# Performance work log

Hardware: AMD Instinct MI355X
Metric: run time of the kernel (lower is better)

Reference implementation:

```python
import jax, jax.numpy as jnp
import numpy as np

N_EMBD = 1024
N_HEAD = 16
HEAD_DIM = N_EMBD // N_HEAD


def setup_inputs() -> dict:
    key = jax.random.key(0)
    ks = jax.random.split(key, 5)
    B, T = 4, 2048
    s = 0.02
    return {
        "x": jax.random.normal(ks[0], (B, T, N_EMBD), dtype=jnp.float32),
        "w_qkv": jax.random.normal(ks[1], (N_EMBD, 3 * N_EMBD), dtype=jnp.float32) * s,
        "b_qkv": jnp.zeros((3 * N_EMBD,), dtype=jnp.float32),
        "w_out": jax.random.normal(ks[2], (N_EMBD, N_EMBD), dtype=jnp.float32) * s,
        "b_out": jnp.zeros((N_EMBD,), dtype=jnp.float32),
    }


def reference(x, w_qkv, b_qkv, w_out, b_out):
    # Eval-mode forward (dropout disabled), matching the torch module's math.
    B, T, C = x.shape
    qkv = x @ w_qkv + b_qkv                      # [B,T,3C]
    q, k, v = jnp.split(qkv, 3, axis=-1)
    def heads(t):
        return t.reshape(B, T, N_HEAD, HEAD_DIM).transpose(0, 2, 1, 3)  # [B,H,T,D]
    q, k, v = heads(q), heads(k), heads(v)
    scores = jnp.einsum("bhtd,bhsd->bhts", q, k) / jnp.sqrt(jnp.float32(HEAD_DIM))
    causal = jnp.tril(jnp.ones((T, T), dtype=bool))
    scores = jnp.where(causal[None, None], scores, -jnp.inf)
    attn = jax.nn.softmax(scores, axis=-1)       # [B,H,T,T]
    y = jnp.einsum("bhts,bhsd->bhtd", attn, v)   # [B,H,T,D]
    y = y.transpose(0, 2, 1, 3).reshape(B, T, C)
    return y @ w_out + b_out
```

## Files before the change

kernel.cpp:

```cpp
#include <hip/hip_runtime.h>
#include <hip/hip_bf16.h>

#define TSEQ 2048
#define CEMB 1024

typedef __attribute__((ext_vector_type(8))) short bf16x8;
typedef __attribute__((ext_vector_type(4))) float f32x4;
typedef __attribute__((ext_vector_type(16))) float f32x16;
typedef __attribute__((ext_vector_type(4))) int i32x4;

__device__ __forceinline__ unsigned short f2bf(float f){
  return __builtin_bit_cast(unsigned short, __float2bfloat16(f));
}

__global__ void k_cvt_bf16(const float* __restrict__ in, unsigned short* __restrict__ out, int n4){
  int i = blockIdx.x * blockDim.x + threadIdx.x;
  if (i >= n4) return;
  const float4 v = reinterpret_cast<const float4*>(in)[i];
  ushort4 o;
  o.x = f2bf(v.x); o.y = f2bf(v.y); o.z = f2bf(v.z); o.w = f2bf(v.w);
  reinterpret_cast<ushort4*>(out)[i] = o;
}

__global__ void k_transpose_bf16(const float* __restrict__ w, unsigned short* __restrict__ wT, int K, int N){
  __shared__ unsigned short tile[32][33];
  const int n0 = blockIdx.x * 32, k0 = blockIdx.y * 32;
  const int tx = threadIdx.x & 31, ty = threadIdx.x >> 5;
  #pragma unroll
  for (int r = 0; r < 4; ++r){
    int k = ty * 4 + r;
    tile[k][tx] = f2bf(w[(size_t)(k0 + k) * N + n0 + tx]);
  }
  __syncthreads();
  #pragma unroll
  for (int r = 0; r < 4; ++r){
    int n = ty * 4 + r;
    wT[(size_t)(n0 + n) * K + k0 + tx] = tile[tx][n];
  }
}

__global__ __launch_bounds__(256) void k_vT(const unsigned short* __restrict__ qkv,
                                            unsigned short* __restrict__ vT){
  __shared__ __align__(16) unsigned short tile[64*64];
  const int tid = threadIdx.x;
  const int bh = blockIdx.x;
  const int t0 = blockIdx.y * 64;
  const int b = bh >> 4, h = bh & 15;
  const int lt = tid >> 3, seg = tid & 7;
  #pragma unroll
  for (int r = 0; r < 2; ++r){
    const int t = lt + 32*r;
    const i32x4 v = *(const i32x4*)&qkv[((size_t)(b*TSEQ + t0 + t))*3072 + 2048 + h*64 + seg*8];
    const int slot = seg ^ (t & 7) ^ (t >> 3);
    *(i32x4*)((char*)tile + t*128 + slot*16) = v;
  }
  __syncthreads();
  const int w = tid >> 6, lane = tid & 63;
  const int tseg = lane & 7;
  #pragma unroll
  for (int r = 0; r < 2; ++r){
    const int d = w*8 + (lane>>3) + 32*r;
    unsigned int wd[4];
    #pragma unroll
    for (int jp = 0; jp < 4; ++jp){
      unsigned int lo, hi;
      #pragma unroll
      for (int e = 0; e < 2; ++e){
        const int j = jp*2 + e;
        const int t = tseg*8 + j;
        const int byteoff = t*128 + ((2*d) ^ (((j ^ tseg) & 7) << 4));
        const unsigned int val = *(const unsigned short*)((const char*)tile + byteoff);
        if (e == 0) lo = val; else hi = val;
      }
      wd[jp] = lo | (hi << 16);
    }
    i32x4 o4; o4[0]=wd[0]; o4[1]=wd[1]; o4[2]=wd[2]; o4[3]=wd[3];
    *(i32x4*)&vT[((size_t)bh*64 + d)*2048 + t0 + tseg*8] = o4;
  }
}

template<bool OUT_BF16>
__global__ __launch_bounds__(256) void k_gemm_bt(
    const unsigned short* __restrict__ A,
    const unsigned short* __restrict__ Bt,
    const float* __restrict__ bias,
    void* __restrict__ Cout, int M, int N, int K)
{
  __shared__ __align__(16) unsigned short As[128*32];
  __shared__ __align__(16) unsigned short Bs[128*32];
  const int tid = threadIdx.x;
  const int lane = tid & 63, w = tid >> 6;
  const int wr = w >> 1, wc = w & 1;
  const int l15 = lane & 15, l4 = lane >> 4;

  const unsigned nwg = gridDim.x * gridDim.y;
  unsigned lin = blockIdx.y * gridDim.x + blockIdx.x;
  {
    const unsigned qq = nwg >> 3, rr = nwg & 7;
    const unsigned xcd = lin & 7, loc = lin >> 3;
    lin = (xcd < rr ? xcd * (qq + 1) : rr * (qq + 1) + (xcd - rr) * qq) + loc;
  }
  const int m0 = (int)(lin / gridDim.x) * 128;
  const int n0 = (int)(lin % gridDim.x) * 128;

  const unsigned short* Ag = A + (size_t)(m0 + (tid >> 2)) * K + (tid & 3) * 8;
  const unsigned short* Bg = Bt + (size_t)(n0 + (tid >> 2)) * K + (tid & 3) * 8;

  f32x4 acc[4][4] = {};

  for (int kk = 0; kk < K; kk += 32){
    #pragma unroll
    for (int rd = 0; rd < 2; ++rd){
      __builtin_amdgcn_global_load_lds(
        (const __attribute__((address_space(1))) void*)(Ag + kk + (size_t)rd * 64 * K),
        (__attribute__((address_space(3))) void*)&As[(rd * 256 + w * 64) * 8],
        16, 0, 0);
      __builtin_amdgcn_global_load_lds(
        (const __attribute__((address_space(1))) void*)(Bg + kk + (size_t)rd * 64 * K),
        (__attribute__((address_space(3))) void*)&Bs[(rd * 256 + w * 64) * 8],
        16, 0, 0);
    }
    __syncthreads();
    bf16x8 af[4], bfr[4];
    #pragma unroll
    for (int m = 0; m < 4; ++m)
      af[m] = *(const bf16x8*)&As[(wr*64 + m*16 + l15) * 32 + l4*8];
    #pragma unroll
    for (int n = 0; n < 4; ++n)
      bfr[n] = *(const bf16x8*)&Bs[(wc*64 + n*16 + l15) * 32 + l4*8];
    #pragma unroll
    for (int m = 0; m < 4; ++m){
      #pragma unroll
      for (int n = 0; n < 4; ++n)
        acc[m][n] = __builtin_amdgcn_mfma_f32_16x16x32_bf16(af[m], bfr[n], acc[m][n], 0, 0, 0);
    }
    __syncthreads();
  }

  float bv[4];
  #pragma unroll
  for (int n = 0; n < 4; ++n) bv[n] = bias[n0 + wc*64 + n*16 + l15];

  #pragma unroll
  for (int m = 0; m < 4; ++m){
    const int row = m0 + wr*64 + m*16 + l4*4;
    #pragma unroll
    for (int n = 0; n < 4; ++n){
      const int col = n0 + wc*64 + n*16 + l15;
      #pragma unroll
      for (int r = 0; r < 4; ++r){
        float v = acc[m][n][r] + bv[n];
        if (OUT_BF16)
          ((unsigned short*)Cout)[(size_t)(row + r) * N + col] = f2bf(v);
        else
          ((float*)Cout)[(size_t)(row + r) * N + col] = v;
      }
    }
  }
}

__global__ __launch_bounds__(512, 4) void k_attn(
    const unsigned short* __restrict__ qkv,
    const unsigned short* __restrict__ vT,
    unsigned short* __restrict__ y)
{
  __shared__ __align__(16) char Ksm[2][8192];
  __shared__ __align__(16) char Vsm[2][8192];
  __shared__ float Ls[8][32];

  const int tid = threadIdx.x, lane = tid & 63, w = tid >> 6;
  const int q31 = lane & 31, hi = lane >> 5;
  const int bh = blockIdx.x, p = blockIdx.y;
  const int g = w >> 2, wl = w & 3;
  const int myt = g ? (15 - p) : p;
  const int b = bh >> 4, h = bh & 15;
  const size_t rowB = (size_t)b * TSEQ;

  const int wq0 = myt*128 + 32*wl, qg = wq0 + q31;
  const int nkt_my = 2*myt + 2;
  const int nktB  = 2*(15 - p) + 2;

  const float sc = 0.18033688011112042f;

  bf16x8 qf[4];
  {
    const unsigned short* qp = qkv + (rowB + qg) * 3072 + h * 64;
    #pragma unroll
    for (int c4 = 0; c4 < 4; ++c4){
      bf16x8 v = *(const bf16x8*)(qp + c4*16 + hi*8);
      #pragma unroll
      for (int j = 0; j < 8; ++j){
        const unsigned int bits = ((unsigned int)(unsigned short)v[j]) << 16;
        v[j] = (short)f2bf(__builtin_bit_cast(float, bits) * sc);
      }
      qf[c4] = v;
    }
  }

  const int kr = lane >> 3, sl = lane & 7, cx = sl ^ kr;
  const unsigned short* kgbase = qkv + (rowB + w*8 + kr) * 3072 + 1024 + h*64 + cx*8;
  const unsigned short* vgbase = vT + ((size_t)bh*64 + w*8 + kr) * 2048 + cx*8;

  #define STAGE(ktile, buf)                                                          \
    do {                                                                             \
      __builtin_amdgcn_global_load_lds(                                              \
        (const __attribute__((address_space(1))) void*)(kgbase + (size_t)(ktile)*64*3072), \
        (__attribute__((address_space(3))) void*)(&Ksm[buf][0] + w*1024), 16, 0, 0); \
      __builtin_amdgcn_global_load_lds(                                              \
        (const __attribute__((address_space(1))) void*)(vgbase + (ktile)*64),        \
        (__attribute__((address_space(3))) void*)(&Vsm[buf][0] + w*1024), 16, 0, 0); \
    } while (0)

  f32x16 O[2] = {};
  float l = 0.f;

  STAGE(0, 0);
  __syncthreads();

  int cbuf = 0;
  for (int kt = 0; kt < nktB; ++kt){
    if (kt + 1 < nktB) STAGE(kt + 1, cbuf ^ 1);

    if (kt < nkt_my){
      const char* kb = Ksm[cbuf];
      const char* vb = Vsm[cbuf];
      const bool domask = (kt*64 + 63 > wq0);
      #pragma unroll
      for (int sub = 0; sub < 2; ++sub){
        f32x16 S = {};
        __builtin_amdgcn_s_setprio(1);
        #pragma unroll
        for (int c4 = 0; c4 < 4; ++c4){
          const bf16x8 kf = *(const bf16x8*)(kb + (sub*32 + q31)*128
                                + ((((c4<<1)|hi) ^ (q31 & 7)) << 4));
          S = __builtin_amdgcn_mfma_f32_32x32x16_bf16(kf, qf[c4], S, 0, 0, 0);
        }
        __builtin_amdgcn_s_setprio(0);
        if (domask){
          #pragma unroll
          for (int r = 0; r < 16; ++r){
            const int kg = kt*64 + sub*32 + (r&3) + 8*(r>>2) + 4*hi;
            if (kg > qg) S[r] = -1e30f;
          }
        }
        float ps = 0.f;
        #pragma unroll
        for (int r = 0; r < 16; ++r){
          S[r] = __builtin_amdgcn_exp2f(S[r]);
          ps += S[r];
        }
        l += ps;
        bf16x8 paf[2];
        #pragma unroll
        for (int kc = 0; kc < 2; ++kc){
          const int e = kc * 8;
          unsigned int a, bb, cc, dd;
          asm("v_cvt_pk_bf16_f32 %0, %1, %2" : "=v"(a)  : "v"(S[e+0]), "v"(S[e+1]));
          asm("v_cvt_pk_bf16_f32 %0, %1, %2" : "=v"(bb) : "v"(S[e+4]), "v"(S[e+5]));
          asm("v_cvt_pk_bf16_f32 %0, %1, %2" : "=v"(cc) : "v"(S[e+2]), "v"(S[e+3]));
          asm("v_cvt_pk_bf16_f32 %0, %1, %2" : "=v"(dd) : "v"(S[e+6]), "v"(S[e+7]));
          asm volatile("v_permlane32_swap_b32 %0, %1" : "+v"(a),  "+v"(bb));
          asm volatile("v_permlane32_swap_b32 %0, %1" : "+v"(cc), "+v"(dd));
          i32x4 pwv; pwv[0] = (int)a; pwv[1] = (int)cc; pwv[2] = (int)bb; pwv[3] = (int)dd;
          paf[kc] = __builtin_bit_cast(bf16x8, pwv);
        }
        __builtin_amdgcn_s_setprio(1);
        #pragma unroll
        for (int kc = 0; kc < 2; ++kc){
          #pragma unroll
          for (int dblk = 0; dblk < 2; ++dblk){
            const int dr = dblk*32 + q31;
            const bf16x8 vf = *(const bf16x8*)(vb + dr*128
                                  + ((((sub<<2)|(kc<<1)|hi) ^ (dr & 7)) << 4));
            O[dblk] = __builtin_amdgcn_mfma_f32_32x32x16_bf16(paf[kc], vf, O[dblk], 0, 0, 0);
          }
        }
        __builtin_amdgcn_s_setprio(0);
      }
    }

    __syncthreads();
    cbuf ^= 1;
  }

  {
    const float lc = l + __shfl_xor(l, 32);
    if (lane < 32) Ls[w][lane] = 1.0f / lc;
  }
  __syncthreads();

  #pragma unroll
  for (int r = 0; r < 16; ++r){
    const int qloc = (r&3) + 8*(r>>2) + 4*hi;
    const float inv = Ls[w][qloc];
    const size_t row = rowB + wq0 + qloc;
    #pragma unroll
    for (int dblk = 0; dblk < 2; ++dblk)
      y[row * CEMB + h*64 + dblk*32 + q31] = f2bf(O[dblk][r] * inv);
  }
  #undef STAGE
}

extern "C" void kernel_launch(void* const* d_in, const int* in_sizes, int n_in,
                              void* d_out, int out_size, void* d_ws, size_t ws_size,
                              hipStream_t stream)
{
  const float* x     = (const float*)d_in[0];
  const float* w_qkv = (const float*)d_in[1];
  const float* b_qkv = (const float*)d_in[2];
  const float* w_out = (const float*)d_in[3];
  const float* b_out = (const float*)d_in[4];
  float* out = (float*)d_out;

  char* ws = (char*)d_ws;
  unsigned short* xb    = (unsigned short*)(ws);
  unsigned short* vTb   = (unsigned short*)(ws);
  unsigned short* qkvb  = (unsigned short*)(ws + (16u<<20));
  unsigned short* yb    = (unsigned short*)(ws + (64u<<20));
  unsigned short* wqkvT = (unsigned short*)(ws + (80u<<20));
  unsigned short* woutT = (unsigned short*)(ws + (86u<<20));

  const int M = 4 * TSEQ;

  k_cvt_bf16<<<(M * CEMB / 4 + 255) / 256, 256, 0, stream>>>(x, xb, M * CEMB / 4);
  k_transpose_bf16<<<dim3(3072/32, 1024/32), 256, 0, stream>>>(w_qkv, wqkvT, 1024, 3072);
  k_transpose_bf16<<<dim3(1024/32, 1024/32), 256, 0, stream>>>(w_out, woutT, 1024, 1024);

  k_gemm_bt<true ><<<dim3(3072/128, M/128), 256, 0, stream>>>(xb, wqkvT, b_qkv, qkvb, M, 3072, 1024);
  k_vT<<<dim3(64, TSEQ/64), 256, 0, stream>>>(qkvb, vTb);
  k_attn<<<dim3(4 * 16, 8), 512, 0, stream>>>(qkvb, vTb, yb);
  k_gemm_bt<false><<<dim3(1024/128, M/128), 256, 0, stream>>>(yb, woutT, b_out, out, M, 1024, 1024);
}
```

Before: 177.6 us.

## Add 256x256-tile pipelined GEMM kernel for the QKV projection

Adds a new GEMM kernel with 256x256 output tiles, 512 threads and a 128 KB double-buffered LDS using XOR-swizzled rows. It stages global loads directly into LDS while MFMAs run, using explicit waitcnt, barriers and setprio. It replaces the 128x128 GEMM for the QKV projection to get more operand reuse and overlap loads with compute. The cost is a large LDS footprint that limits occupancy and only 384 workgroups for 256 CUs, which risks tail imbalance.

```diff
diff --git a/kernel.cpp b/kernel.cpp
--- a/kernel.cpp
+++ b/kernel.cpp
@@ -12,6 +12,14 @@
 __device__ __forceinline__ unsigned short f2bf(float f){
   return __builtin_bit_cast(unsigned short, __float2bfloat16(f));
 }
+
+__device__ __forceinline__ f32x4 MFMA16(bf16x8 a, bf16x8 b, f32x4 c){
+  return __builtin_amdgcn_mfma_f32_16x16x32_bf16(a, b, c, 0, 0, 0);
+}
+
+#define GLDS(src, dst) __builtin_amdgcn_global_load_lds( \
+      (const __attribute__((address_space(1))) void*)(src), \
+      (__attribute__((address_space(3))) void*)(dst), 16, 0, 0)
 
 __global__ void k_cvt_bf16(const float* __restrict__ in, unsigned short* __restrict__ out, int n4){
   int i = blockIdx.x * blockDim.x + threadIdx.x;
@@ -111,14 +119,8 @@
   for (int kk = 0; kk < K; kk += 32){
     #pragma unroll
     for (int rd = 0; rd < 2; ++rd){
-      __builtin_amdgcn_global_load_lds(
-        (const __attribute__((address_space(1))) void*)(Ag + kk + (size_t)rd * 64 * K),
-        (__attribute__((address_space(3))) void*)&As[(rd * 256 + w * 64) * 8],
-        16, 0, 0);
-      __builtin_amdgcn_global_load_lds(
-        (const __attribute__((address_space(1))) void*)(Bg + kk + (size_t)rd * 64 * K),
-        (__attribute__((address_space(3))) void*)&Bs[(rd * 256 + w * 64) * 8],
-        16, 0, 0);
+      GLDS(Ag + kk + (size_t)rd * 64 * K, &As[(rd * 256 + w * 64) * 8]);
+      GLDS(Bg + kk + (size_t)rd * 64 * K, &Bs[(rd * 256 + w * 64) * 8]);
     }
     __syncthreads();
     bf16x8 af[4], bfr[4];
@@ -132,7 +134,7 @@
     for (int m = 0; m < 4; ++m){
       #pragma unroll
       for (int n = 0; n < 4; ++n)
-        acc[m][n] = __builtin_amdgcn_mfma_f32_16x16x32_bf16(af[m], bfr[n], acc[m][n], 0, 0, 0);
+        acc[m][n] = MFMA16(af[m], bfr[n], acc[m][n]);
     }
     __syncthreads();
   }
@@ -147,6 +149,150 @@
     #pragma unroll
     for (int n = 0; n < 4; ++n){
       const int col = n0 + wc*64 + n*16 + l15;
+      #pragma unroll
+      for (int r = 0; r < 4; ++r){
+        float v = acc[m][n][r] + bv[n];
+        if (OUT_BF16)
+          ((unsigned short*)Cout)[(size_t)(row + r) * N + col] = f2bf(v);
+        else
+          ((float*)Cout)[(size_t)(row + r) * N + col] = v;
+      }
+    }
+  }
+}
+
+template<bool OUT_BF16>
+__global__ __launch_bounds__(512, 2) void k_gemm256(
+    const unsigned short* __restrict__ A,
+    const unsigned short* __restrict__ Bt,
+    const float* __restrict__ bias,
+    void* __restrict__ Cout, int M, int N, int K)
+{
+  __shared__ __align__(16) char smem[131072];
+  const int tid = threadIdx.x;
+  const int lane = tid & 63, w = tid >> 6;
+  const int wm = w >> 2, wn = w & 3;
+  const int l15 = lane & 15, l4 = lane >> 4;
+  const int x7 = l15 & 7;
+
+  unsigned lin = blockIdx.x;
+  {
+    const unsigned nwg = gridDim.x;
+    const unsigned qq = nwg >> 3, rr = nwg & 7;
+    const unsigned xcd = lin & 7, loc = lin >> 3;
+    lin = (xcd < rr ? xcd * (qq + 1) : rr * (qq + 1) + (xcd - rr) * qq) + loc;
+  }
+  const unsigned ntn = (unsigned)N >> 8;
+  const int m0 = (int)(lin / ntn) << 8;
+  const int n0 = (int)(lin % ntn) << 8;
+
+  const int srow = lane >> 3;
+  const int scx  = (lane & 7) ^ srow;
+  const unsigned short* Ag = A  + (size_t)(m0 + w*8 + srow) * K + scx * 8;
+  const unsigned short* Bg = Bt + (size_t)(n0 + w*8 + srow) * K + scx * 8;
+  char* const As0 = smem + (w << 10);
+  char* const Bs0 = smem + 65536 + (w << 10);
+
+  auto stageA = [&](int buf, int kt){
+    const unsigned short* s = Ag + kt*64;
+    char* d = As0 + buf*32768;
+    #pragma unroll
+    for (int i = 0; i < 4; ++i) GLDS(s + (size_t)(i*64)*K, d + i*8192);
+  };
+  auto stageB = [&](int buf, int kt){
+    const unsigned short* s = Bg + kt*64;
+    char* d = Bs0 + buf*32768;
+    #pragma unroll
+    for (int i = 0; i < 4; ++i) GLDS(s + (size_t)(i*64)*K, d + i*8192);
+  };
+
+  const int arow = wm*128 + l15;
+  const int brow = wn*64  + l15;
+  auto rdA = [&](int buf, int m, int ks)->bf16x8 {
+    return *(const bf16x8*)(smem + buf*32768 + (arow + m*16)*128 + (((ks*4 + l4) ^ x7) << 4));
+  };
+  auto rdB = [&](int buf, int n, int ks)->bf16x8 {
+    return *(const bf16x8*)(smem + 65536 + buf*32768 + (brow + n*16)*128 + (((ks*4 + l4) ^ x7) << 4));
+  };
+
+  f32x4 acc[8][4] = {};
+  const int NIT = K >> 7;
+
+  stageA(0, 0); stageB(0, 0);
+  stageA(1, 1); stageB(1, 1);
+  asm volatile("s_waitcnt vmcnt(8)" ::: "memory");
+  __builtin_amdgcn_s_barrier();
+  asm volatile("" ::: "memory");
+
+  for (int it = 0; it < NIT; ++it){
+    const bool more = (it + 1 < NIT);
+    #pragma unroll
+    for (int half = 0; half < 2; ++half){
+      const int buf = half;
+      bf16x8 bfr[4][2], af1[4][2], af2[4][2];
+      #pragma unroll
+      for (int n = 0; n < 4; ++n){ bfr[n][0] = rdB(buf, n, 0); bfr[n][1] = rdB(buf, n, 1); }
+      #pragma unroll
+      for (int m = 0; m < 4; ++m){ af1[m][0] = rdA(buf, m, 0); af1[m][1] = rdA(buf, m, 1); }
+      __builtin_amdgcn_s_setprio(1);
+      #pragma unroll
+      for (int m = 0; m < 4; ++m)
+        #pragma unroll
+        for (int n = 0; n < 2; ++n)
+          #pragma unroll
+          for (int ks = 0; ks < 2; ++ks)
+            acc[m][n] = MFMA16(af1[m][ks], bfr[n][ks], acc[m][n]);
+      __builtin_amdgcn_s_setprio(0);
+      #pragma unroll
+      for (int m = 0; m < 4; ++m){ af2[m][0] = rdA(buf, m+4, 0); af2[m][1] = rdA(buf, m+4, 1); }
+      __builtin_amdgcn_s_setprio(1);
+      #pragma unroll
+      for (int m = 0; m < 4; ++m)
+        #pragma unroll
+        for (int n = 2; n < 4; ++n)
+          #pragma unroll
+          for (int ks = 0; ks < 2; ++ks)
+            acc[m][n] = MFMA16(af1[m][ks], bfr[n][ks], acc[m][n]);
+      __builtin_amdgcn_s_setprio(0);
+      __builtin_amdgcn_s_setprio(1);
+      #pragma unroll
+      for (int m = 0; m < 4; ++m)
+        #pragma unroll
+        for (int n = 2; n < 4; ++n)
+          #pragma unroll
+          for (int ks = 0; ks < 2; ++ks)
+            acc[m+4][n] = MFMA16(af2[m][ks], bfr[n][ks], acc[m+4][n]);
+      __builtin_amdgcn_s_setprio(0);
+      asm volatile("s_waitcnt lgkmcnt(0)" ::: "memory");
+      __builtin_amdgcn_s_barrier();
+      asm volatile("" ::: "memory");
+      if (more){ stageA(buf, 2*it + half + 2); stageB(buf, 2*it + half + 2); }
+      __builtin_amdgcn_s_setprio(1);
+      #pragma unroll
+      for (int m = 0; m < 4; ++m)
+        #pragma unroll
+        for (int n = 0; n < 2; ++n)
+          #pragma unroll
+          for (int ks = 0; ks < 2; ++ks)
+            acc[m+4][n] = MFMA16(af2[m][ks], bfr[n][ks], acc[m+4][n]);
+      __builtin_amdgcn_s_setprio(0);
+      if (more) asm volatile("s_waitcnt vmcnt(8)" ::: "memory");
+      else      asm volatile("s_waitcnt vmcnt(0)" ::: "memory");
+      __builtin_amdgcn_s_barrier();
+      asm volatile("" ::: "memory");
+    }
+  }
+
+  float bv[4];
+  #pragma unroll
+  for (int n = 0; n < 4; ++n) bv[n] = bias[n0 + wn*64 + n*16 + l15];
+
+  #pragma unroll
+  for (int m = 0; m < 8; ++m){
+    const int row = m0 + wm*128 + m*16 + l4*4;
+    #pragma unroll
+    for (int n = 0; n < 4; ++n){
+      const int col = n0 + wn*64 + n*16 + l15;
       #pragma unroll
       for (int r = 0; r < 4; ++r){
         float v = acc[m][n][r] + bv[n];
@@ -203,12 +349,8 @@
 
   #define STAGE(ktile, buf)                                                          \
     do {                                                                             \
-      __builtin_amdgcn_global_load_lds(                                              \
-        (const __attribute__((address_space(1))) void*)(kgbase + (size_t)(ktile)*64*3072), \
-        (__attribute__((address_space(3))) void*)(&Ksm[buf][0] + w*1024), 16, 0, 0); \
-      __builtin_amdgcn_global_load_lds(                                              \
-        (const __attribute__((address_space(1))) void*)(vgbase + (ktile)*64),        \
-        (__attribute__((address_space(3))) void*)(&Vsm[buf][0] + w*1024), 16, 0, 0); \
+      GLDS(kgbase + (size_t)(ktile)*64*3072, &Ksm[buf][0] + w*1024);                 \
+      GLDS(vgbase + (ktile)*64,              &Vsm[buf][0] + w*1024);                 \
     } while (0)
 
   f32x16 O[2] = {};
@@ -326,7 +468,7 @@
   k_transpose_bf16<<<dim3(3072/32, 1024/32), 256, 0, stream>>>(w_qkv, wqkvT, 1024, 3072);
   k_transpose_bf16<<<dim3(1024/32, 1024/32), 256, 0, stream>>>(w_out, woutT, 1024, 1024);
 
-  k_gemm_bt<true ><<<dim3(3072/128, M/128), 256, 0, stream>>>(xb, wqkvT, b_qkv, qkvb, M, 3072, 1024);
+  k_gemm256<true><<<dim3((M/256) * (3072/256)), 512, 0, stream>>>(xb, wqkvT, b_qkv, qkvb, M, 3072, 1024);
   k_vT<<<dim3(64, TSEQ/64), 256, 0, stream>>>(qkvb, vTb);
   k_attn<<<dim3(4 * 16, 8), 512, 0, stream>>>(qkvb, vTb, yb);
   k_gemm_bt<false><<<dim3(1024/128, M/128), 256, 0, stream>>>(yb, woutT, b_out, out, M, 1024, 1024);
```

After: 167.2 us. 5.8% less time.
